# Kernel tuning notes

Hardware: AMD Instinct MI355X
Metric: run time of the kernel (lower is better)

The kernel has to match this reference:

```python
import jax, jax.numpy as jnp
import numpy as np

# kernel hyperparameters (base_params)
NUGGET = 0.001
REG_LAMBDA = 0.01
FIT_L, FIT_SIGMA = 1.0, 1.0
MMD_L, MMD_SIGMA = 1.0, 1.0
N, D = 4096, 4


def rbf_gram(X1, X2, l, sigma):
    # [N1,N2] radial kernel: sigma^2 * exp(-||x-x'||^2 / (2 l^2)), vectorized
    sq = (jnp.sum(X1 * X1, axis=1)[:, None]
          + jnp.sum(X2 * X2, axis=1)[None, :]
          - 2.0 * (X1 @ X2.T))
    sq = jnp.maximum(sq, 0.0)
    return (sigma * sigma) * jnp.exp(-sq / (2.0 * l * l))


def setup_inputs() -> dict:
    key = jax.random.key(0)
    kx, ky, kz = jax.random.split(key, 3)
    X = jax.random.normal(kx, (N, D), dtype=jnp.float32)
    Y = jax.random.normal(ky, (N, D), dtype=jnp.float32)
    Z = Y + 0.1 * jax.random.normal(kz, (N, D), dtype=jnp.float32)  # Z init'd from Y, perturbed
    return {"X": X, "Y": Y, "Z": Z}


def reference(X, Y, Z):
    # fit_kXX and its nugget-regularized inverse (precomputed in __init__)
    fit_kXX = rbf_gram(X, X, FIT_L, FIT_SIGMA)
    fit_kXX_inv = jnp.linalg.inv(fit_kXX + NUGGET * jnp.eye(X.shape[0], dtype=X.dtype))

    # loss_fit_z: ||k_ZZ||_F^2 - 2 ||k_ZY||_F^2  (torch matrix norm = Frobenius)
    k_ZZ = rbf_gram(Z, Z, MMD_L, MMD_SIGMA)
    k_ZY = rbf_gram(Z, Y, MMD_L, MMD_SIGMA)
    loss_fit = jnp.sum(k_ZZ * k_ZZ) - 2.0 * jnp.sum(k_ZY * k_ZY)

    # loss_reg_z: reg_lambda * trace(Z^T fit_kXX_inv Z)
    loss_reg = REG_LAMBDA * jnp.sum(Z * (fit_kXX_inv @ Z))

    return loss_fit + loss_reg
```

## Files before the change

### kernel.cpp

```cpp
#include <hip/hip_runtime.h>


#define NN   4096
#define LDA  4100
#define OFF_W ((size_t)NN*LDA)
#define OFF_ACC_B ((OFF_W + (size_t)NN*4)*4)

__device__ __forceinline__ float rdlane(float v, int l){
    return __int_as_float(__builtin_amdgcn_readlane(__float_as_int(v), l));
}

__global__ void k_build_A(const float* __restrict__ X, float* __restrict__ A){
    const int i  = blockIdx.y;
    const int j0 = (blockIdx.x*256 + threadIdx.x)*4;
    const float4 xi = *(const float4*)(X + (size_t)i*4);
    float out[4];
#pragma unroll
    for (int s=0;s<4;s++){
        const float4 xj = *(const float4*)(X + (size_t)(j0+s)*4);
        float d0=xi.x-xj.x, d1=xi.y-xj.y, d2=xi.z-xj.z, d3=xi.w-xj.w;
        float sq = d0*d0+d1*d1+d2*d2+d3*d3;
        float v  = __expf(-0.5f*sq);
        if (i == j0+s) v += 0.001f;
        out[s]=v;
    }
    *(float4*)(A + (size_t)i*LDA + j0) = make_float4(out[0],out[1],out[2],out[3]);
}

__device__ void wave_chol64(const float* Dm, float* __restrict__ A, int k2){
    const int lane = threadIdx.x & 63;
    float row[64];
#pragma unroll
    for (int q=0;q<16;q++){
        float4 v = *(const float4*)(Dm + lane*68 + q*4);
        row[q*4]=v.x; row[q*4+1]=v.y; row[q*4+2]=v.z; row[q*4+3]=v.w;
    }
#pragma unroll
    for (int j=0;j<64;j++){
        float d  = rdlane(row[j], j);
        float sd = sqrtf(d);
        float inv= 1.0f/sd;
        float v  = (lane==j)? sd : row[j]*inv;
        row[j] = v;
#pragma unroll
        for (int c=j+1;c<64;c++){
            float lc = rdlane(v, c);
            row[c] -= v*lc;
        }
    }
#pragma unroll
    for (int q=0;q<16;q++)
        *(float4*)(A + (size_t)(k2+lane)*LDA + k2 + q*4) =
            make_float4(row[q*4],row[q*4+1],row[q*4+2],row[q*4+3]);
}

__global__ __launch_bounds__(256) void k_step(float* __restrict__ A, float* __restrict__ W,
                                              const float* __restrict__ Z, int s){
    __shared__ float S[8704];
    const int tid = threadIdx.x;
    const int bid = blockIdx.x;
    const int k2   = (s+1)*64;
    const int T    = 63 - s;
    const int T2   = (T+1)>>1;
    const int nT2  = T2*(T2+1)/2;
    const int kcol = s*64;

    if (bid == 0){
        float* P  = S;
        float* Dm = S + 4352;
        if (s >= 0){
#pragma unroll
            for (int it=0; it<4; ++it){
                int idx = tid + it*256;
                int r = idx>>4, q = idx&15;
                float4 v = *(const float4*)(A + (size_t)(k2+r)*LDA + kcol + q*4);
                P[(q*4+0)*68+r]=v.x; P[(q*4+1)*68+r]=v.y;
                P[(q*4+2)*68+r]=v.z; P[(q*4+3)*68+r]=v.w;
            }
            __syncthreads();
            const int tx = tid&15, ty = tid>>4;
            float acc[4][4]={};
#pragma unroll 8
            for (int t=0;t<64;t++){
                float4 a = *(const float4*)&P[t*68 + ty*4];
                float4 b = *(const float4*)&P[t*68 + tx*4];
                acc[0][0]+=a.x*b.x; acc[0][1]+=a.x*b.y; acc[0][2]+=a.x*b.z; acc[0][3]+=a.x*b.w;
                acc[1][0]+=a.y*b.x; acc[1][1]+=a.y*b.y; acc[1][2]+=a.y*b.z; acc[1][3]+=a.y*b.w;
                acc[2][0]+=a.z*b.x; acc[2][1]+=a.z*b.y; acc[2][2]+=a.z*b.z; acc[2][3]+=a.z*b.w;
                acc[3][0]+=a.w*b.x; acc[3][1]+=a.w*b.y; acc[3][2]+=a.w*b.z; acc[3][3]+=a.w*b.w;
            }
#pragma unroll
            for (int i=0;i<4;i++){
                float4 c = *(const float4*)(A + (size_t)(k2+ty*4+i)*LDA + k2 + tx*4);
                c.x-=acc[i][0]; c.y-=acc[i][1]; c.z-=acc[i][2]; c.w-=acc[i][3];
                *(float4*)&Dm[(ty*4+i)*68 + tx*4] = c;
            }
        } else {
#pragma unroll
            for (int it=0; it<4; ++it){
                int idx = tid + it*256;
                int r = idx>>4, q = idx&15;
                float4 v = *(const float4*)(A + (size_t)(k2+r)*LDA + k2 + q*4);
                *(float4*)&Dm[r*68 + q*4] = v;
            }
        }
        __syncthreads();
        if (tid < 64) wave_chol64(Dm, A, k2);
    } else if (bid <= nT2){
        int t2 = bid-1;
        int bi = (int)((sqrtf(8.f*(float)t2+1.f)-1.f)*0.5f);
        while ((bi+1)*(bi+2)/2 <= t2) ++bi;
        while (bi*(bi+1)/2 > t2) --bi;
        const int bj = t2 - bi*(bi+1)/2;
        const int r0 = k2 + bi*128, c0 = k2 + bj*128;
        const int diag = (bi==bj);
        float* Sa = S;
        float* Sb = diag ? S : (S + 4224);
        const int tx = tid&15, ty = tid>>4;
        float acc[8][8]={};
        for (int kk=0; kk<2; ++kk){
            const int kb = kcol + kk*32;
#pragma unroll
            for (int it=0; it<4; ++it){
                int idx = tid + it*256;
                int row = idx>>3, q = idx&7;
                int rl = r0+row; if (rl>4095) rl=4095;
                float4 v = *(const float4*)(A + (size_t)rl*LDA + kb + q*4);
                Sa[(q*4+0)*132+row]=v.x; Sa[(q*4+1)*132+row]=v.y;
                Sa[(q*4+2)*132+row]=v.z; Sa[(q*4+3)*132+row]=v.w;
            }
            if (!diag){
#pragma unroll
                for (int it=0; it<4; ++it){
                    int idx = tid + it*256;
                    int row = idx>>3, q = idx&7;
                    int cl = c0+row; if (cl>4095) cl=4095;
                    float4 v = *(const float4*)(A + (size_t)cl*LDA + kb + q*4);
                    Sb[(q*4+0)*132+row]=v.x; Sb[(q*4+1)*132+row]=v.y;
                    Sb[(q*4+2)*132+row]=v.z; Sb[(q*4+3)*132+row]=v.w;
                }
            }
            __syncthreads();
#pragma unroll 4
            for (int t=0;t<32;t++){
                float4 a0 = *(const float4*)&Sa[t*132 + ty*8];
                float4 a1 = *(const float4*)&Sa[t*132 + ty*8 + 4];
                float4 b0 = *(const float4*)&Sb[t*132 + tx*8];
                float4 b1 = *(const float4*)&Sb[t*132 + tx*8 + 4];
                float av[8]={a0.x,a0.y,a0.z,a0.w,a1.x,a1.y,a1.z,a1.w};
                float bv[8]={b0.x,b0.y,b0.z,b0.w,b1.x,b1.y,b1.z,b1.w};
#pragma unroll
                for (int i=0;i<8;i++)
#pragma unroll
                    for (int j=0;j<8;j++) acc[i][j] += av[i]*bv[j];
            }
            __syncthreads();
        }
#pragma unroll
        for (int i=0;i<8;i++){
            const int r = r0 + ty*8 + i;
            if (r > 4095) continue;
#pragma unroll
            for (int jq=0;jq<2;jq++){
                const int c = c0 + tx*8 + jq*4;
                if (c > 4095) continue;
                if (r < k2+64 && c < k2+64) continue;
                float* p = A + (size_t)r*LDA + c;
                float4 cv = *(float4*)p;
                cv.x -= acc[i][jq*4+0]; cv.y -= acc[i][jq*4+1];
                cv.z -= acc[i][jq*4+2]; cv.w -= acc[i][jq*4+3];
                *(float4*)p = cv;
            }
        }
    } else {
        const int wu = bid - 1 - nT2;
        const int rrow = k2 + wu*64;
        float* Lt = S;
        float* Ws = S + 4352;
#pragma unroll
        for (int it=0; it<4; ++it){
            int idx = tid + it*256;
            int r = idx>>4, q = idx&15;
            float4 v = *(const float4*)(A + (size_t)(rrow+r)*LDA + kcol + q*4);
            *(float4*)&Lt[r*68 + q*4] = v;
        }
        if (tid < 64){
            float4 v = *(const float4*)(W + (size_t)(kcol+tid)*4);
            *(float4*)&Ws[tid*4] = v;
        }
        __syncthreads();
        if (tid < 64){
            const float* wsrc = (s==0) ? (Z + (size_t)(rrow+tid)*4) : (W + (size_t)(rrow+tid)*4);
            float4 w = *(const float4*)wsrc;
#pragma unroll 8
            for (int t=0;t<64;t++){
                float l = Lt[tid*68 + t];
                float4 x = *(const float4*)&Ws[t*4];
                w.x -= l*x.x; w.y -= l*x.y; w.z -= l*x.z; w.w -= l*x.w;
            }
            *(float4*)(W + (size_t)(rrow+tid)*4) = w;
        }
    }
}

__global__ __launch_bounds__(256) void k_trsm2(float* __restrict__ A, float* __restrict__ W,
                                               const float* __restrict__ Z, int s){
    __shared__ float Ld[64*68];
    __shared__ float dinv[64];
    const int tid = threadIdx.x;
    const int s0  = s*64;
#pragma unroll
    for (int it=0; it<4; ++it){
        int idx = tid + it*256;
        int r = idx>>4, q = idx&15;
        float4 v = *(const float4*)(A + (size_t)(s0+r)*LDA + s0 + q*4);
        *(float4*)&Ld[r*68 + q*4] = v;
    }
    __syncthreads();
    if (tid < 64) dinv[tid] = 1.0f/Ld[tid*68 + tid];
    __syncthreads();

    const int nRB = (63-s+3)>>2;
    if ((int)blockIdx.x < nRB){
        const int row = s0 + 64 + blockIdx.x*256 + tid;
        const int rl  = row>4095 ? 4095 : row;
        float x[64];
        const float* src = A + (size_t)rl*LDA + s0;
#pragma unroll
        for (int q=0;q<16;q++){
            float4 v = *(const float4*)(src + q*4);
            x[q*4]=v.x; x[q*4+1]=v.y; x[q*4+2]=v.z; x[q*4+3]=v.w;
        }
#pragma unroll
        for (int c=0;c<64;c++){
            float xc = x[c]*dinv[c];
            x[c] = xc;
#pragma unroll
            for (int t=c+1;t<64;t++) x[t] -= xc*Ld[t*68 + c];
        }
        if (row < 4096){
            float* dst = A + (size_t)row*LDA + s0;
#pragma unroll
            for (int q=0;q<16;q++)
                *(float4*)(dst + q*4) = make_float4(x[q*4],x[q*4+1],x[q*4+2],x[q*4+3]);
        }
    } else {
        if (tid < 64){
            const int lane = tid;
            const float* wsrc = (s==0) ? (Z + (size_t)(s0+lane)*4) : (W + (size_t)(s0+lane)*4);
            float4 wv = *(const float4*)wsrc;
            float w0=wv.x, w1=wv.y, w2=wv.z, w3=wv.w;
#pragma unroll
            for (int j=0;j<64;j++){
                if (lane==j){ float dj=dinv[j]; w0*=dj; w1*=dj; w2*=dj; w3*=dj; }
                float b0=__shfl(w0,j), b1=__shfl(w1,j), b2=__shfl(w2,j), b3=__shfl(w3,j);
                float l = Ld[lane*68 + j];
                if (lane>j){ w0-=l*b0; w1-=l*b1; w2-=l*b2; w3-=l*b3; }
            }
            *(float4*)(W + (size_t)(s0+lane)*4) = make_float4(w0,w1,w2,w3);
        }
    }
}

__global__ void k_lossfit(const float* __restrict__ Z, const float* __restrict__ Y,
                          double* __restrict__ acc){
    const int tid=threadIdx.x;
    const int i0=blockIdx.x*8;
    double s=0.0;
    for (int ii=0;ii<8;ii++){
        const float4 zi = *(const float4*)(Z + (size_t)(i0+ii)*4);
        for (int j=tid;j<NN;j+=256){
            float4 zj = *(const float4*)(Z + (size_t)j*4);
            float4 yj = *(const float4*)(Y + (size_t)j*4);
            float d0=zi.x-zj.x, d1=zi.y-zj.y, d2=zi.z-zj.z, d3=zi.w-zj.w;
            float dzz = d0*d0+d1*d1+d2*d2+d3*d3;
            d0=zi.x-yj.x; d1=zi.y-yj.y; d2=zi.z-yj.z; d3=zi.w-yj.w;
            float dzy = d0*d0+d1*d1+d2*d2+d3*d3;
            s += (double)(__expf(-dzz) - 2.f*__expf(-dzy));
        }
    }
    for (int o=32;o;o>>=1) s += __shfl_down(s,o);
    __shared__ double ps[4];
    if ((tid&63)==0) ps[tid>>6]=s;
    __syncthreads();
    if (tid==0) atomicAdd(acc, ps[0]+ps[1]+ps[2]+ps[3]);
}

__global__ void k_zero(double* acc){ if (threadIdx.x==0) acc[0]=0.0; }

__global__ void k_finish(const float* __restrict__ W, const double* __restrict__ acc,
                         float* __restrict__ out){
    const int tid=threadIdx.x;
    double s=0.0;
    for (int r=tid;r<NN;r+=256){
        float4 v=*(const float4*)(W+(size_t)r*4);
        s += (double)v.x*v.x+(double)v.y*v.y+(double)v.z*v.z+(double)v.w*v.w;
    }
    for (int o=32;o;o>>=1) s += __shfl_down(s,o);
    __shared__ double ps[4];
    if ((tid&63)==0) ps[tid>>6]=s;
    __syncthreads();
    if (tid==0) out[0] = (float)(acc[0] + 0.01*(ps[0]+ps[1]+ps[2]+ps[3]));
}

extern "C" void kernel_launch(void* const* d_in, const int* in_sizes, int n_in,
                              void* d_out, int out_size, void* d_ws, size_t ws_size,
                              hipStream_t stream){
    const float* X=(const float*)d_in[0];
    const float* Y=(const float*)d_in[1];
    const float* Z=(const float*)d_in[2];
    float* ws   = (float*)d_ws;
    float* A    = ws;
    float* W    = ws + OFF_W;
    double* acc = (double*)((char*)d_ws + OFF_ACC_B);

    if (ws_size < OFF_ACC_B + 64) return;

    k_zero   <<<1,64,0,stream>>>(acc);
    k_lossfit<<<512,256,0,stream>>>(Z,Y,acc);
    k_build_A<<<dim3(NN/1024,NN),256,0,stream>>>(X,A);

    k_step<<<1,256,0,stream>>>(A,W,Z,-1);
    for (int s=0;s<64;s++){
        const int T = 63-s;
        const int nRB = (T+3)>>2;
        k_trsm2<<<nRB+1,256,0,stream>>>(A,W,Z,s);
        if (s < 63){
            const int T2 = (T+1)>>1;
            const int nT2 = T2*(T2+1)/2;
            k_step<<<nT2+1+T,256,0,stream>>>(A,W,Z,s);
        }
    }
    k_finish<<<1,256,0,stream>>>(W,acc,(float*)d_out);
}
```

Measured before the change: 3.492 ms.

## Restructure blocked Cholesky into panel updates plus deferred 256-wide trailing updates

Result: slower. 3.625 ms (+3.8%).

```diff
diff --git a/kernel.cpp b/kernel.cpp
--- a/kernel.cpp
+++ b/kernel.cpp
@@ -1,13 +1,40 @@
 #include <hip/hip_runtime.h>
 
 
-#define NN   4096
-#define LDA  4100
-#define OFF_W ((size_t)NN*LDA)
-#define OFF_ACC_B ((OFF_W + (size_t)NN*4)*4)
+#define NN 4096
+#define LDA 4100
+#define OFF_W   ((size_t)NN*LDA)
+#define OFF_ACC (OFF_W + (size_t)NN*4)
 
 __device__ __forceinline__ float rdlane(float v, int l){
     return __int_as_float(__builtin_amdgcn_readlane(__float_as_int(v), l));
+}
+
+__device__ void wave_chol64(const float* Dm, float* __restrict__ A, int h){
+    const int lane = threadIdx.x & 63;
+    float row[64];
+#pragma unroll
+    for (int q=0;q<16;q++){
+        float4 v = *(const float4*)(Dm + lane*68 + q*4);
+        row[q*4]=v.x; row[q*4+1]=v.y; row[q*4+2]=v.z; row[q*4+3]=v.w;
+    }
+#pragma unroll
+    for (int j=0;j<64;j++){
+        float d  = rdlane(row[j], j);
+        float sd = sqrtf(d);
+        float inv= 1.0f/sd;
+        float v  = (lane==j)? sd : row[j]*inv;
+        row[j] = v;
+#pragma unroll
+        for (int c=j+1;c<64;c++){
+            float lc = rdlane(v, c);
+            row[c] -= v*lc;
+        }
+    }
+#pragma unroll
+    for (int q=0;q<16;q++)
+        *(float4*)(A + (size_t)(h+lane)*LDA + h + q*4) =
+            make_float4(row[q*4],row[q*4+1],row[q*4+2],row[q*4+3]);
 }
 
 __global__ void k_build_A(const float* __restrict__ X, float* __restrict__ A){
@@ -27,192 +54,35 @@
     *(float4*)(A + (size_t)i*LDA + j0) = make_float4(out[0],out[1],out[2],out[3]);
 }
 
-__device__ void wave_chol64(const float* Dm, float* __restrict__ A, int k2){
-    const int lane = threadIdx.x & 63;
-    float row[64];
-#pragma unroll
-    for (int q=0;q<16;q++){
-        float4 v = *(const float4*)(Dm + lane*68 + q*4);
-        row[q*4]=v.x; row[q*4+1]=v.y; row[q*4+2]=v.z; row[q*4+3]=v.w;
-    }
-#pragma unroll
-    for (int j=0;j<64;j++){
-        float d  = rdlane(row[j], j);
-        float sd = sqrtf(d);
-        float inv= 1.0f/sd;
-        float v  = (lane==j)? sd : row[j]*inv;
-        row[j] = v;
-#pragma unroll
-        for (int c=j+1;c<64;c++){
-            float lc = rdlane(v, c);
-            row[c] -= v*lc;
-        }
-    }
-#pragma unroll
-    for (int q=0;q<16;q++)
-        *(float4*)(A + (size_t)(k2+lane)*LDA + k2 + q*4) =
-            make_float4(row[q*4],row[q*4+1],row[q*4+2],row[q*4+3]);
-}
-
-__global__ __launch_bounds__(256) void k_step(float* __restrict__ A, float* __restrict__ W,
-                                              const float* __restrict__ Z, int s){
-    __shared__ float S[8704];
+__global__ void k_init(const float* __restrict__ Z, float* __restrict__ W,
+                       double* __restrict__ acc){
+    const int i = blockIdx.x*256+threadIdx.x;
+    ((float4*)W)[i] = ((const float4*)Z)[i];
+    if (blockIdx.x==0 && threadIdx.x==0) acc[0]=0.0;
+}
+
+__global__ __launch_bounds__(256) void k_chol0(float* __restrict__ A){
+    __shared__ float Dm[64*68];
     const int tid = threadIdx.x;
-    const int bid = blockIdx.x;
-    const int k2   = (s+1)*64;
-    const int T    = 63 - s;
-    const int T2   = (T+1)>>1;
-    const int nT2  = T2*(T2+1)/2;
-    const int kcol = s*64;
-
-    if (bid == 0){
-        float* P  = S;
-        float* Dm = S + 4352;
-        if (s >= 0){
-#pragma unroll
-            for (int it=0; it<4; ++it){
-                int idx = tid + it*256;
-                int r = idx>>4, q = idx&15;
-                float4 v = *(const float4*)(A + (size_t)(k2+r)*LDA + kcol + q*4);
-                P[(q*4+0)*68+r]=v.x; P[(q*4+1)*68+r]=v.y;
-                P[(q*4+2)*68+r]=v.z; P[(q*4+3)*68+r]=v.w;
-            }
-            __syncthreads();
-            const int tx = tid&15, ty = tid>>4;
-            float acc[4][4]={};
-#pragma unroll 8
-            for (int t=0;t<64;t++){
-                float4 a = *(const float4*)&P[t*68 + ty*4];
-                float4 b = *(const float4*)&P[t*68 + tx*4];
-                acc[0][0]+=a.x*b.x; acc[0][1]+=a.x*b.y; acc[0][2]+=a.x*b.z; acc[0][3]+=a.x*b.w;
-                acc[1][0]+=a.y*b.x; acc[1][1]+=a.y*b.y; acc[1][2]+=a.y*b.z; acc[1][3]+=a.y*b.w;
-                acc[2][0]+=a.z*b.x; acc[2][1]+=a.z*b.y; acc[2][2]+=a.z*b.z; acc[2][3]+=a.z*b.w;
-                acc[3][0]+=a.w*b.x; acc[3][1]+=a.w*b.y; acc[3][2]+=a.w*b.z; acc[3][3]+=a.w*b.w;
-            }
-#pragma unroll
-            for (int i=0;i<4;i++){
-                float4 c = *(const float4*)(A + (size_t)(k2+ty*4+i)*LDA + k2 + tx*4);
-                c.x-=acc[i][0]; c.y-=acc[i][1]; c.z-=acc[i][2]; c.w-=acc[i][3];
-                *(float4*)&Dm[(ty*4+i)*68 + tx*4] = c;
-            }
-        } else {
-#pragma unroll
-            for (int it=0; it<4; ++it){
-                int idx = tid + it*256;
-                int r = idx>>4, q = idx&15;
-                float4 v = *(const float4*)(A + (size_t)(k2+r)*LDA + k2 + q*4);
-                *(float4*)&Dm[r*68 + q*4] = v;
-            }
-        }
-        __syncthreads();
-        if (tid < 64) wave_chol64(Dm, A, k2);
-    } else if (bid <= nT2){
-        int t2 = bid-1;
-        int bi = (int)((sqrtf(8.f*(float)t2+1.f)-1.f)*0.5f);
-        while ((bi+1)*(bi+2)/2 <= t2) ++bi;
-        while (bi*(bi+1)/2 > t2) --bi;
-        const int bj = t2 - bi*(bi+1)/2;
-        const int r0 = k2 + bi*128, c0 = k2 + bj*128;
-        const int diag = (bi==bj);
-        float* Sa = S;
-        float* Sb = diag ? S : (S + 4224);
-        const int tx = tid&15, ty = tid>>4;
-        float acc[8][8]={};
-        for (int kk=0; kk<2; ++kk){
-            const int kb = kcol + kk*32;
-#pragma unroll
-            for (int it=0; it<4; ++it){
-                int idx = tid + it*256;
-                int row = idx>>3, q = idx&7;
-                int rl = r0+row; if (rl>4095) rl=4095;
-                float4 v = *(const float4*)(A + (size_t)rl*LDA + kb + q*4);
-                Sa[(q*4+0)*132+row]=v.x; Sa[(q*4+1)*132+row]=v.y;
-                Sa[(q*4+2)*132+row]=v.z; Sa[(q*4+3)*132+row]=v.w;
-            }
-            if (!diag){
-#pragma unroll
-                for (int it=0; it<4; ++it){
-                    int idx = tid + it*256;
-                    int row = idx>>3, q = idx&7;
-                    int cl = c0+row; if (cl>4095) cl=4095;
-                    float4 v = *(const float4*)(A + (size_t)cl*LDA + kb + q*4);
-                    Sb[(q*4+0)*132+row]=v.x; Sb[(q*4+1)*132+row]=v.y;
-                    Sb[(q*4+2)*132+row]=v.z; Sb[(q*4+3)*132+row]=v.w;
-                }
-            }
-            __syncthreads();
-#pragma unroll 4
-            for (int t=0;t<32;t++){
-                float4 a0 = *(const float4*)&Sa[t*132 + ty*8];
-                float4 a1 = *(const float4*)&Sa[t*132 + ty*8 + 4];
-                float4 b0 = *(const float4*)&Sb[t*132 + tx*8];
-                float4 b1 = *(const float4*)&Sb[t*132 + tx*8 + 4];
-                float av[8]={a0.x,a0.y,a0.z,a0.w,a1.x,a1.y,a1.z,a1.w};
-                float bv[8]={b0.x,b0.y,b0.z,b0.w,b1.x,b1.y,b1.z,b1.w};
-#pragma unroll
-                for (int i=0;i<8;i++)
-#pragma unroll
-                    for (int j=0;j<8;j++) acc[i][j] += av[i]*bv[j];
-            }
-            __syncthreads();
-        }
-#pragma unroll
-        for (int i=0;i<8;i++){
-            const int r = r0 + ty*8 + i;
-            if (r > 4095) continue;
-#pragma unroll
-            for (int jq=0;jq<2;jq++){
-                const int c = c0 + tx*8 + jq*4;
-                if (c > 4095) continue;
-                if (r < k2+64 && c < k2+64) continue;
-                float* p = A + (size_t)r*LDA + c;
-                float4 cv = *(float4*)p;
-                cv.x -= acc[i][jq*4+0]; cv.y -= acc[i][jq*4+1];
-                cv.z -= acc[i][jq*4+2]; cv.w -= acc[i][jq*4+3];
-                *(float4*)p = cv;
-            }
-        }
-    } else {
-        const int wu = bid - 1 - nT2;
-        const int rrow = k2 + wu*64;
-        float* Lt = S;
-        float* Ws = S + 4352;
-#pragma unroll
-        for (int it=0; it<4; ++it){
-            int idx = tid + it*256;
-            int r = idx>>4, q = idx&15;
-            float4 v = *(const float4*)(A + (size_t)(rrow+r)*LDA + kcol + q*4);
-            *(float4*)&Lt[r*68 + q*4] = v;
-        }
-        if (tid < 64){
-            float4 v = *(const float4*)(W + (size_t)(kcol+tid)*4);
-            *(float4*)&Ws[tid*4] = v;
-        }
-        __syncthreads();
-        if (tid < 64){
-            const float* wsrc = (s==0) ? (Z + (size_t)(rrow+tid)*4) : (W + (size_t)(rrow+tid)*4);
-            float4 w = *(const float4*)wsrc;
-#pragma unroll 8
-            for (int t=0;t<64;t++){
-                float l = Lt[tid*68 + t];
-                float4 x = *(const float4*)&Ws[t*4];
-                w.x -= l*x.x; w.y -= l*x.y; w.z -= l*x.z; w.w -= l*x.w;
-            }
-            *(float4*)(W + (size_t)(rrow+tid)*4) = w;
-        }
-    }
+#pragma unroll
+    for (int it=0; it<4; ++it){
+        int idx = tid + it*256, r = idx>>4, q = idx&15;
+        float4 v = *(const float4*)(A + (size_t)r*LDA + q*4);
+        *(float4*)&Dm[r*68 + q*4] = v;
+    }
+    __syncthreads();
+    if (tid < 64) wave_chol64(Dm, A, 0);
 }
 
 __global__ __launch_bounds__(256) void k_trsm2(float* __restrict__ A, float* __restrict__ W,
-                                               const float* __restrict__ Z, int s){
+                                               int g){
     __shared__ float Ld[64*68];
     __shared__ float dinv[64];
     const int tid = threadIdx.x;
-    const int s0  = s*64;
+    const int s0  = g*64;
 #pragma unroll
     for (int it=0; it<4; ++it){
-        int idx = tid + it*256;
-        int r = idx>>4, q = idx&15;
+        int idx = tid + it*256, r = idx>>4, q = idx&15;
         float4 v = *(const float4*)(A + (size_t)(s0+r)*LDA + s0 + q*4);
         *(float4*)&Ld[r*68 + q*4] = v;
     }
@@ -220,7 +90,7 @@
     if (tid < 64) dinv[tid] = 1.0f/Ld[tid*68 + tid];
     __syncthreads();
 
-    const int nRB = (63-s+3)>>2;
+    const int nRB = (66-g)>>2;
     if ((int)blockIdx.x < nRB){
         const int row = s0 + 64 + blockIdx.x*256 + tid;
         const int rl  = row>4095 ? 4095 : row;
@@ -247,8 +117,7 @@
     } else {
         if (tid < 64){
             const int lane = tid;
-            const float* wsrc = (s==0) ? (Z + (size_t)(s0+lane)*4) : (W + (size_t)(s0+lane)*4);
-            float4 wv = *(const float4*)wsrc;
+            float4 wv = *(const float4*)(W + (size_t)(s0+lane)*4);
             float w0=wv.x, w1=wv.y, w2=wv.z, w3=wv.w;
 #pragma unroll
             for (int j=0;j<64;j++){
@@ -259,6 +128,209 @@
             }
             *(float4*)(W + (size_t)(s0+lane)*4) = make_float4(w0,w1,w2,w3);
         }
+    }
+}
+
+__global__ __launch_bounds__(256) void k_pupd(float* __restrict__ A, float* __restrict__ W,
+                                              int g){
+    __shared__ float Sh[2*4352];
+    const int tid = threadIdx.x;
+    const int g64 = g*64;
+    const int i = g&3, ncols = 3-i;
+    int idx = blockIdx.x;
+    int c_blk=-1, r_blk=-1;
+#pragma unroll
+    for (int cc=0; cc<3; ++cc){
+        if (cc < ncols && c_blk < 0){
+            int cb = g+1+cc, cnt = 64-cb;
+            if (idx < cnt){ c_blk=cb; r_blk=cb+idx; }
+            else idx -= cnt;
+        }
+    }
+    const int tx = tid&15, ty = tid>>4;
+
+    if (c_blk >= 0){
+        float* PrT = Sh;
+        float* PcT = (r_blk==c_blk) ? Sh : (Sh + 4352);
+        const int r0 = r_blk*64, c0 = c_blk*64;
+#pragma unroll
+        for (int it=0; it<4; ++it){
+            int ix = tid + it*256, r = ix>>4, q = ix&15;
+            float4 v = *(const float4*)(A + (size_t)(r0+r)*LDA + g64 + q*4);
+            PrT[(q*4+0)*68+r]=v.x; PrT[(q*4+1)*68+r]=v.y;
+            PrT[(q*4+2)*68+r]=v.z; PrT[(q*4+3)*68+r]=v.w;
+        }
+        if (r_blk != c_blk){
+#pragma unroll
+            for (int it=0; it<4; ++it){
+                int ix = tid + it*256, r = ix>>4, q = ix&15;
+                float4 v = *(const float4*)(A + (size_t)(c0+r)*LDA + g64 + q*4);
+                PcT[(q*4+0)*68+r]=v.x; PcT[(q*4+1)*68+r]=v.y;
+                PcT[(q*4+2)*68+r]=v.z; PcT[(q*4+3)*68+r]=v.w;
+            }
+        }
+        __syncthreads();
+        float acc[4][4]={};
+#pragma unroll 8
+        for (int t=0;t<64;t++){
+            float4 a = *(const float4*)&PrT[t*68 + ty*4];
+            float4 b = *(const float4*)&PcT[t*68 + tx*4];
+            acc[0][0]+=a.x*b.x; acc[0][1]+=a.x*b.y; acc[0][2]+=a.x*b.z; acc[0][3]+=a.x*b.w;
+            acc[1][0]+=a.y*b.x; acc[1][1]+=a.y*b.y; acc[1][2]+=a.y*b.z; acc[1][3]+=a.y*b.w;
+            acc[2][0]+=a.z*b.x; acc[2][1]+=a.z*b.y; acc[2][2]+=a.z*b.z; acc[2][3]+=a.z*b.w;
+            acc[3][0]+=a.w*b.x; acc[3][1]+=a.w*b.y; acc[3][2]+=a.w*b.z; acc[3][3]+=a.w*b.w;
+        }
+        if (r_blk==c_blk && c_blk==g+1){
+            float* Dm = Sh + 4352;
+            __syncthreads();
+#pragma unroll
+            for (int ii=0;ii<4;ii++){
+                float4 c = *(const float4*)(A + (size_t)(r0+ty*4+ii)*LDA + c0 + tx*4);
+                c.x-=acc[ii][0]; c.y-=acc[ii][1]; c.z-=acc[ii][2]; c.w-=acc[ii][3];
+                *(float4*)&Dm[(ty*4+ii)*68 + tx*4] = c;
+            }
+            __syncthreads();
+            if (tid < 64) wave_chol64(Dm, A, r0);
+        } else {
+#pragma unroll
+            for (int ii=0;ii<4;ii++){
+                float* p = A + (size_t)(r0+ty*4+ii)*LDA + c0 + tx*4;
+                float4 cv = *(float4*)p;
+                cv.x-=acc[ii][0]; cv.y-=acc[ii][1]; cv.z-=acc[ii][2]; cv.w-=acc[ii][3];
+                *(float4*)p = cv;
+            }
+        }
+    } else {
+        const int wr0 = (g+1+idx)*64;
+        float* Lt = Sh;
+        float* Ws = Sh + 4352;
+#pragma unroll
+        for (int it=0; it<4; ++it){
+            int ix = tid + it*256, r = ix>>4, q = ix&15;
+            float4 v = *(const float4*)(A + (size_t)(wr0+r)*LDA + g64 + q*4);
+            *(float4*)&Lt[r*68 + q*4] = v;
+        }
+        if (tid < 64) *(float4*)&Ws[tid*4] = *(const float4*)(W + (size_t)(g64+tid)*4);
+        __syncthreads();
+        const int row = tid>>2, cw = tid&3;
+        float s = 0.f;
+#pragma unroll 16
+        for (int t=0;t<64;t++) s += Lt[row*68+t]*Ws[t*4+cw];
+        float* wp = W + (size_t)(wr0+row)*4 + cw;
+        *wp = *wp - s;
+    }
+}
+
+__global__ __launch_bounds__(256) void k_upd256(float* __restrict__ A, int S){
+    __shared__ float S_[8704];
+    const int tid = threadIdx.x;
+    const int k0 = S*256, base = k0+256;
+    const int T2 = (4096-base)>>7;
+    const int nT2 = T2*(T2+1)/2;
+    const int tx = tid&15, ty = tid>>4;
+
+    if ((int)blockIdx.x == nT2){
+        float* PT = S_;
+        float* Dm = S_ + 4352;
+        float acc[4][4]={};
+        for (int kk=0; kk<4; ++kk){
+            __syncthreads();
+#pragma unroll
+            for (int it=0; it<4; ++it){
+                int ix = tid + it*256, r = ix>>4, q = ix&15;
+                float4 v = *(const float4*)(A + (size_t)(base+r)*LDA + k0 + kk*64 + q*4);
+                PT[(q*4+0)*68+r]=v.x; PT[(q*4+1)*68+r]=v.y;
+                PT[(q*4+2)*68+r]=v.z; PT[(q*4+3)*68+r]=v.w;
+            }
+            __syncthreads();
+#pragma unroll 8
+            for (int t=0;t<64;t++){
+                float4 a = *(const float4*)&PT[t*68 + ty*4];
+                float4 b = *(const float4*)&PT[t*68 + tx*4];
+                acc[0][0]+=a.x*b.x; acc[0][1]+=a.x*b.y; acc[0][2]+=a.x*b.z; acc[0][3]+=a.x*b.w;
+                acc[1][0]+=a.y*b.x; acc[1][1]+=a.y*b.y; acc[1][2]+=a.y*b.z; acc[1][3]+=a.y*b.w;
+                acc[2][0]+=a.z*b.x; acc[2][1]+=a.z*b.y; acc[2][2]+=a.z*b.z; acc[2][3]+=a.z*b.w;
+                acc[3][0]+=a.w*b.x; acc[3][1]+=a.w*b.y; acc[3][2]+=a.w*b.z; acc[3][3]+=a.w*b.w;
+            }
+        }
+        __syncthreads();
+#pragma unroll
+        for (int ii=0;ii<4;ii++){
+            float4 c = *(const float4*)(A + (size_t)(base+ty*4+ii)*LDA + base + tx*4);
+            c.x-=acc[ii][0]; c.y-=acc[ii][1]; c.z-=acc[ii][2]; c.w-=acc[ii][3];
+            *(float4*)&Dm[(ty*4+ii)*68 + tx*4] = c;
+        }
+        __syncthreads();
+        if (tid < 64) wave_chol64(Dm, A, base);
+        return;
+    }
+
+    float* Sa = S_;
+    float* Sb = S_ + 4224;
+    int t2 = blockIdx.x;
+    int bi = (int)((sqrtf(8.f*(float)t2+1.f)-1.f)*0.5f);
+    while ((bi+1)*(bi+2)/2 <= t2) ++bi;
+    while (bi*(bi+1)/2 > t2) --bi;
+    const int bj = t2 - bi*(bi+1)/2;
+    const int r0 = base + bi*128, c0 = base + bj*128;
+    const bool dg = (bi==bj);
+    const float* Sbp = dg ? Sa : Sb;
+    int row_[4], q_[4];
+#pragma unroll
+    for (int it=0;it<4;++it){ int ix=tid+it*256; row_[it]=ix>>3; q_[it]=ix&7; }
+    float4 ra[4], rb[4];
+#pragma unroll
+    for (int it=0;it<4;++it){
+        ra[it] = *(const float4*)(A + (size_t)(r0+row_[it])*LDA + k0 + q_[it]*4);
+        if (!dg) rb[it] = *(const float4*)(A + (size_t)(c0+row_[it])*LDA + k0 + q_[it]*4);
+    }
+    float acc[8][8]={};
+    for (int kk=0;kk<8;++kk){
+        __syncthreads();
+#pragma unroll
+        for (int it=0;it<4;++it){
+            Sa[(q_[it]*4+0)*132+row_[it]]=ra[it].x; Sa[(q_[it]*4+1)*132+row_[it]]=ra[it].y;
+            Sa[(q_[it]*4+2)*132+row_[it]]=ra[it].z; Sa[(q_[it]*4+3)*132+row_[it]]=ra[it].w;
+            if (!dg){
+                Sb[(q_[it]*4+0)*132+row_[it]]=rb[it].x; Sb[(q_[it]*4+1)*132+row_[it]]=rb[it].y;
+                Sb[(q_[it]*4+2)*132+row_[it]]=rb[it].z; Sb[(q_[it]*4+3)*132+row_[it]]=rb[it].w;
+            }
+        }
+        __syncthreads();
+        if (kk < 7){
+            const int kb = k0 + (kk+1)*32;
+#pragma unroll
+            for (int it=0;it<4;++it){
+                ra[it] = *(const float4*)(A + (size_t)(r0+row_[it])*LDA + kb + q_[it]*4);
+                if (!dg) rb[it] = *(const float4*)(A + (size_t)(c0+row_[it])*LDA + kb + q_[it]*4);
+            }
+        }
+#pragma unroll 4
+        for (int t=0;t<32;++t){
+            float4 a0 = *(const float4*)&Sa[t*132 + ty*8];
+            float4 a1 = *(const float4*)&Sa[t*132 + ty*8 + 4];
+            float4 b0 = *(const float4*)&Sbp[t*132 + tx*8];
+            float4 b1 = *(const float4*)&Sbp[t*132 + tx*8 + 4];
+            float av[8]={a0.x,a0.y,a0.z,a0.w,a1.x,a1.y,a1.z,a1.w};
+            float bv[8]={b0.x,b0.y,b0.z,b0.w,b1.x,b1.y,b1.z,b1.w};
+#pragma unroll
+            for (int ii=0;ii<8;ii++)
+#pragma unroll
+                for (int jj=0;jj<8;jj++) acc[ii][jj] += av[ii]*bv[jj];
+        }
+    }
+#pragma unroll
+    for (int ii=0;ii<8;ii++){
+        const int r = r0 + ty*8 + ii;
+        const int c = c0 + tx*8;
+        if (r < base+64 && c < base+64) continue;
+        float* p = A + (size_t)r*LDA + c;
+        float4 c1 = *(float4*)p;
+        c1.x-=acc[ii][0]; c1.y-=acc[ii][1]; c1.z-=acc[ii][2]; c1.w-=acc[ii][3];
+        *(float4*)p = c1;
+        float4 c2 = *(float4*)(p+4);
+        c2.x-=acc[ii][4]; c2.y-=acc[ii][5]; c2.z-=acc[ii][6]; c2.w-=acc[ii][7];
+        *(float4*)(p+4) = c2;
     }
 }
 
@@ -286,8 +358,6 @@
     if (tid==0) atomicAdd(acc, ps[0]+ps[1]+ps[2]+ps[3]);
 }
 
-__global__ void k_zero(double* acc){ if (threadIdx.x==0) acc[0]=0.0; }
-
 __global__ void k_finish(const float* __restrict__ W, const double* __restrict__ acc,
                          float* __restrict__ out){
     const int tid=threadIdx.x;
@@ -312,24 +382,29 @@
     float* ws   = (float*)d_ws;
     float* A    = ws;
     float* W    = ws + OFF_W;
-    double* acc = (double*)((char*)d_ws + OFF_ACC_B);
-
-    if (ws_size < OFF_ACC_B + 64) return;
-
-    k_zero   <<<1,64,0,stream>>>(acc);
-    k_lossfit<<<512,256,0,stream>>>(Z,Y,acc);
-    k_build_A<<<dim3(NN/1024,NN),256,0,stream>>>(X,A);
-
-    k_step<<<1,256,0,stream>>>(A,W,Z,-1);
-    for (int s=0;s<64;s++){
-        const int T = 63-s;
-        const int nRB = (T+3)>>2;
-        k_trsm2<<<nRB+1,256,0,stream>>>(A,W,Z,s);
-        if (s < 63){
-            const int T2 = (T+1)>>1;
+    double* acc = (double*)(ws + OFF_ACC);
+
+    if (ws_size < (OFF_ACC)*sizeof(float) + 16) return;
+
+    k_init   <<<16,256,0,stream>>>(Z, W, acc);
+    k_build_A<<<dim3(NN/1024,NN),256,0,stream>>>(X, A);
+    k_lossfit<<<512,256,0,stream>>>(Z, Y, acc);
+    k_chol0  <<<1,256,0,stream>>>(A);
+
+    for (int g=0; g<64; ++g){
+        const int nRB = (66-g)>>2;
+        k_trsm2<<<nRB+1,256,0,stream>>>(A, W, g);
+        const int i = g&3, ncols = 3-i;
+        int ntile = 0;
+        for (int cc=0; cc<ncols; ++cc) ntile += 64-(g+1+cc);
+        const int nW = 63-g;
+        if (ntile+nW > 0) k_pupd<<<ntile+nW,256,0,stream>>>(A, W, g);
+        if (i==3 && g<63){
+            const int S = g>>2;
+            const int T2 = (4096-(S+1)*256)>>7;
             const int nT2 = T2*(T2+1)/2;
-            k_step<<<nT2+1+T,256,0,stream>>>(A,W,Z,s);
-        }
-    }
-    k_finish<<<1,256,0,stream>>>(W,acc,(float*)d_out);
-}
+            k_upd256<<<nT2+1,256,0,stream>>>(A, S);
+        }
+    }
+    k_finish<<<1,256,0,stream>>>(W, acc, (float*)d_out);
+}
```
